# Performance work log

Measured on AMD Instinct MI355X. Metric: run time of the kernel, lower is better.

Reference implementation:

```python
import jax, jax.numpy as jnp
import numpy as np

EPS = 1e-5
CIN = [3, 24, 48, 96, 192]
COUT = [24, 48, 96, 192, 384]
P = 512
NUM_CLASSES = 101
FC_IN = 384 * 16 * 3 * 3  # 55296


def _poly_layer(x, proj, alpha, gamma, beta):
    # x: (B, C, D, H, W)
    B, C, D, H, W = x.shape
    # im2col: 3x3x3 patches with zero padding 1 -> (B, C*27, D, H, W)
    patches = jax.lax.conv_general_dilated_patches(
        x, filter_shape=(3, 3, 3), window_strides=(1, 1, 1),
        padding=[(1, 1), (1, 1), (1, 1)])
    patches = jnp.moveaxis(patches, 1, -1)  # (B, D, H, W, C*27)
    ws = jnp.einsum('bdhwk,pk->bdhwp', patches, proj)      # projector GEMM
    out = jnp.einsum('bdhwp,po->bdhwo', ws, alpha)         # alpha GEMM
    out = jnp.maximum(1.0 + out, 0.0)                      # clamp(1+x, min=0)
    out = jnp.moveaxis(out, -1, 1)                         # (B, O, D, H, W)
    # MaxPool3d kernel/stride (1,2,2)
    out = jax.lax.reduce_window(out, -jnp.inf, jax.lax.max,
                                (1, 1, 1, 2, 2), (1, 1, 1, 2, 2), 'VALID')
    # BatchNorm3d with batch statistics (train-mode math)
    mean = out.mean(axis=(0, 2, 3, 4), keepdims=True)
    var = out.var(axis=(0, 2, 3, 4), keepdims=True)
    out = (out - mean) * jax.lax.rsqrt(var + EPS)
    out = out * gamma.reshape(1, -1, 1, 1, 1) + beta.reshape(1, -1, 1, 1, 1)
    return out


def setup_inputs() -> dict:
    key = jax.random.key(0)
    keys = jax.random.split(key, 32)
    inp = {'x': jax.random.normal(keys[0], (2, 3, 16, 112, 112), dtype=jnp.float32)}
    ki = 1
    for i in range(5):
        k_feat = CIN[i] * 27
        inp[f'p{i+1}'] = jax.random.normal(keys[ki], (P, k_feat), dtype=jnp.float32) / np.sqrt(k_feat); ki += 1
        inp[f'a{i+1}'] = jax.random.normal(keys[ki], (P, COUT[i]), dtype=jnp.float32) * np.sqrt(2.0 / COUT[i]); ki += 1
        inp[f'g{i+1}'] = jnp.ones((COUT[i],), dtype=jnp.float32)
        inp[f'q{i+1}'] = jnp.zeros((COUT[i],), dtype=jnp.float32)
    inp['w1'] = jax.random.normal(keys[ki], (512, FC_IN), dtype=jnp.float32) * np.sqrt(2.0 / 512); ki += 1
    inp['b1'] = jnp.zeros((512,), dtype=jnp.float32)
    inp['w2'] = jax.random.normal(keys[ki], (256, 512), dtype=jnp.float32) * np.sqrt(2.0 / 256); ki += 1
    inp['b2'] = jnp.zeros((256,), dtype=jnp.float32)
    inp['w3'] = jax.random.normal(keys[ki], (NUM_CLASSES, 256), dtype=jnp.float32) * np.sqrt(2.0 / NUM_CLASSES); ki += 1
    inp['b3'] = jnp.zeros((NUM_CLASSES,), dtype=jnp.float32)
    return inp


def reference(x, p1, a1, g1, q1, p2, a2, g2, q2, p3, a3, g3, q3,
              p4, a4, g4, q4, p5, a5, g5, q5, w1, b1, w2, b2, w3, b3):
    projs = [p1, p2, p3, p4, p5]
    alphas = [a1, a2, a3, a4, a5]
    gammas = [g1, g2, g3, g4, g5]
    betas = [q1, q2, q3, q4, q5]
    h = x
    for i in range(5):
        h = _poly_layer(h, projs[i], alphas[i], gammas[i], betas[i])
    h = h.reshape(h.shape[0], -1)  # (B, 55296)
    h = jax.nn.relu(h @ w1.T + b1)  # dropout = identity (eval)
    h = jax.nn.relu(h @ w2.T + b2)
    logits = h @ w3.T + b3
    return logits
```

## Files before the change

### kernel.cpp

```cpp
#include <hip/hip_runtime.h>

#define EPS_BN 1e-5f

typedef __attribute__((ext_vector_type(8))) short sh8;
typedef __attribute__((ext_vector_type(4))) short sh4;
typedef __attribute__((ext_vector_type(4))) float f32x4;

static const size_t WF_OFF[5] = {0, 1944, 33048, 157464, 655128};
static const size_t PART_OFF = 2645784;
static const size_t PRE_OFF  = 6258456;
static const size_t OUT5_OFF = 8666904;
static const size_t H_OFF    = 8777496;
static const size_t ST_OFF   = 8888088;
static const size_t BNP_OFF  = 8888856;
static const size_t H1_OFF   = 8938008;
static const size_t WS_TOT   = 8939032;
__device__ __align__(256) float g_ws[WS_TOT];

static const size_t XIN_OFF = 0;
static const size_t A1_OFF  = 1871424;
static const size_t A2_OFF  = 4776768;
static const size_t A3_OFF  = 6331968;
static const size_t A4_OFF  = 7216704;
static const size_t AR_TOT  = 7776576;
__device__ __align__(256) unsigned short g_act[AR_TOT];

static const size_t WB_OFF[5] = {0, 4096, 36352, 162304, 659968};
__device__ __align__(256) unsigned short g_wb[2650624];

__device__ inline unsigned short f2bf(float v) {
    unsigned u = __float_as_uint(v);
    return (unsigned short)((u + 0x7fffu + ((u >> 16) & 1u)) >> 16);
}

__global__ __launch_bounds__(256) void init_input(const float* __restrict__ x,
                                                  unsigned short* __restrict__ xp,
                                                  float* __restrict__ bnp,
                                                  int4* __restrict__ zp, int nz)
{
    const int i = blockIdx.x * 256 + threadIdx.x;
    if (i < nz) zp[i] = make_int4(0, 0, 0, 0);
    if (i < 49152) bnp[i] = 0.f;
    if (i >= 2 * 18 * 114 * 114 * 4) return;
    const int c = i & 3;
    int t = i >> 2;
    const int xx = t % 114; t /= 114;
    const int yy = t % 114; t /= 114;
    const int zz = t % 18;
    const int b  = t / 18;
    float v = 0.f;
    if (c < 3 && (unsigned)(zz - 1) < 16u && (unsigned)(yy - 1) < 112u && (unsigned)(xx - 1) < 112u)
        v = x[(((size_t)b * 3 + c) * 16 + (zz - 1)) * 12544 + (yy - 1) * 112 + (xx - 1)];
    xp[i] = f2bf(v);
}

struct FuseArgs {
    const float* proj[5];
    const float* alpha[5];
    float* Wf[5];
    int K[5];
    int CO[5];
    int NT[5];
    int start[6];
};

__global__ __launch_bounds__(256) void fuse_all(FuseArgs a)
{
    __shared__ __align__(16) float sa[16][64];
    __shared__ __align__(16) float sp[16][64];

    int l = 0;
    {
        const int bx = blockIdx.x;
        while (l < 4 && bx >= a.start[l + 1]) ++l;
    }
    const int idx = blockIdx.x - a.start[l];
    const int NT = a.NT[l];
    const int obase = (idx / NT) * 64;
    const int kbase = (idx % NT) * 64;
    const int K = a.K[l], CO = a.CO[l];
    const float* __restrict__ proj  = a.proj[l];
    const float* __restrict__ alpha = a.alpha[l];
    float* __restrict__ Wf = a.Wf[l];

    const int tid = threadIdx.x;
    const int tk = tid & 15, to = tid >> 4;

    const int pp  = tid >> 4;
    const int col = (tid & 15) * 4;
    const int o_st = obase + col;
    const int k_st = kbase + col;
    const bool a_ok  = (o_st < CO);
    const bool p_vec = ((K & 3) == 0) && (k_st + 4 <= K);

    float acc[4][4];
    #pragma unroll
    for (int i = 0; i < 4; ++i)
        #pragma unroll
        for (int j = 0; j < 4; ++j) acc[i][j] = 0.f;

    for (int p0 = 0; p0 < 512; p0 += 16) {
        const float* ap  = alpha + (size_t)(p0 + pp) * CO;
        const float* prp = proj  + (size_t)(p0 + pp) * K;
        float4 va = make_float4(0.f, 0.f, 0.f, 0.f);
        float4 vp = make_float4(0.f, 0.f, 0.f, 0.f);
        if (a_ok) va = *(const float4*)(ap + o_st);
        if (p_vec) {
            vp = *(const float4*)(prp + k_st);
        } else {
            float t4[4];
            #pragma unroll
            for (int j = 0; j < 4; ++j)
                t4[j] = (k_st + j < K) ? prp[k_st + j] : 0.f;
            vp = make_float4(t4[0], t4[1], t4[2], t4[3]);
        }
        *(float4*)&sa[pp][col] = va;
        *(float4*)&sp[pp][col] = vp;
        __syncthreads();
        #pragma unroll
        for (int p = 0; p < 16; ++p) {
            const float4 a4 = *(const float4*)&sa[p][to * 4];
            const float4 b4 = *(const float4*)&sp[p][tk * 4];
            const float aa[4] = {a4.x, a4.y, a4.z, a4.w};
            const float bb[4] = {b4.x, b4.y, b4.z, b4.w};
            #pragma unroll
            for (int i = 0; i < 4; ++i)
                #pragma unroll
                for (int j = 0; j < 4; ++j)
                    acc[i][j] = fmaf(aa[i], bb[j], acc[i][j]);
        }
        __syncthreads();
    }

    #pragma unroll
    for (int i = 0; i < 4; ++i) {
        const int o = obase + to * 4 + i;
        if (o < CO) {
            #pragma unroll
            for (int j = 0; j < 4; ++j) {
                const int kk = kbase + tk * 4 + j;
                if (kk < K) Wf[(size_t)o * K + kk] = acc[i][j];
            }
        }
    }
}

struct ReordArgs {
    const float* Wf[5];
    unsigned short* Wb[5];
    int K[5], CPAD[5], KPAD[5], CO[5];
    int start[6];
};

__global__ __launch_bounds__(256) void reorder_all(ReordArgs a)
{
    int l = 0;
    {
        const int bx = blockIdx.x;
        while (l < 4 && bx >= a.start[l + 1]) ++l;
    }
    const int o = blockIdx.x - a.start[l];
    const int K = a.K[l], CPAD = a.CPAD[l], KPAD = a.KPAD[l], CO = a.CO[l];
    const int tid = threadIdx.x;
    unsigned short* row = a.Wb[l] + (size_t)o * KPAD;
    for (int i = tid; i < KPAD; i += 256) row[i] = 0;
    __syncthreads();
    if (o < CO) {
        const float* wr = a.Wf[l] + (size_t)o * K;
        for (int k = tid; k < K; k += 256) {
            const int c = k / 27, s = k - c * 27;
            row[s * CPAD + c] = f2bf(wr[k]);
        }
    }
}

template<int CPAD, int COUT, int KPAD, int HI, int WI, int HP, int WP, int NBLK, int SPLIT>
__global__ __launch_bounds__(256) void conv_mfma(
    const unsigned short* __restrict__ in, const unsigned short* __restrict__ Wb,
    float* __restrict__ outf, float* __restrict__ part, float* __restrict__ bnp)
{
    constexpr int NT = NBLK / 16;
    constexpr int HI2 = HI + 2, WI2 = WI + 2;
    constexpr bool C8 = (CPAD % 8 == 0);
    constexpr int TABN = C8 ? KPAD / 8 : KPAD / 4;
    constexpr int NSTEP = KPAD / 32 / SPLIT;
    constexpr int MTOT = 2 * 16 * HP * WP * 4;
    constexpr bool BONCE = (NBLK * KPAD * 2 <= 16384);
    constexpr int BROW = BONCE ? (KPAD + 8) : 40;
    constexpr int BS_ELEMS = BONCE ? NBLK * BROW : 2 * NBLK * 40;

    __shared__ __align__(16) unsigned short As[2][128 * 40];
    __shared__ __align__(16) unsigned short Bs[BS_ELEMS];
    __shared__ int tab[TABN];
    __shared__ float bs[(SPLIT == 1) ? 2 * NBLK : 1];

    const int tid = threadIdx.x;
    const int lane = tid & 63;
    const int wv = tid >> 6;
    const int blk_m = blockIdx.x;
    const int oc0 = blockIdx.y * NBLK;
    const int kc = (SPLIT > 1) ? blockIdx.z : 0;

    for (int i = tid; i < TABN; i += 256) {
        const int k = i * (C8 ? 8 : 4);
        const int s = k / CPAD, c = k % CPAD;
        tab[i] = (s < 27) ? ((((s / 9) * HI2 + (s % 9) / 3) * WI2 + (s % 3)) * CPAD + c) : -1;
    }

    if constexpr (BONCE) {
        for (int i = tid; i < NBLK * KPAD / 8; i += 256) {
            const int r = i / (KPAD / 8), kk = i - r * (KPAD / 8);
            *(sh8*)&Bs[r * BROW + kk * 8] = *(const sh8*)&Wb[(size_t)(oc0 + r) * KPAD + kk * 8];
        }
    }

    const int srow = tid >> 1;
    const int half = tid & 1;
    const int m_g = blk_m * 128 + srow;
    {
    }
    const int pooled_s = m_g >> 2, sub_s = m_g & 3;
    const int pw_g = pooled_s % WP;
    const int ph_g = (pooled_s / WP) % HP;
    const int d_g  = (pooled_s / (WP * HP)) & 15;
    const int b_g  = pooled_s / (WP * HP * 16);
    const int h_g = 2 * ph_g + (sub_s >> 1);
    const int w_g = 2 * pw_g + (sub_s & 1);
    const size_t base_m = ((((size_t)b_g * 18 + d_g) * HI2 + h_g) * WI2 + w_g) * CPAD;

    const int brow = tid >> 2, bcc = tid & 3;
    const bool bload = (tid < NBLK * 4);

    f32x4 acc[2][NT];
    #pragma unroll
    for (int mf = 0; mf < 2; ++mf)
        #pragma unroll
        for (int i = 0; i < NT; ++i) acc[mf][i] = (f32x4){0.f, 0.f, 0.f, 0.f};

    const int k_begin = kc * NSTEP * 32;

    sh8 aA0, aA1;
    sh4 aP0, aP1, aP2, aP3;
    sh8 brg;

    __syncthreads();

    {
        const int k0 = k_begin;
        if constexpr (C8) {
            const int o0 = tab[(k0 >> 3) + half * 2];
            const int o1 = tab[(k0 >> 3) + half * 2 + 1];
            aA0 = (sh8){0, 0, 0, 0, 0, 0, 0, 0};
            aA1 = (sh8){0, 0, 0, 0, 0, 0, 0, 0};
            if (o0 >= 0) aA0 = *(const sh8*)(in + base_m + o0);
            if (o1 >= 0) aA1 = *(const sh8*)(in + base_m + o1);
            *(sh8*)&As[0][srow * 40 + (half * 2) * 8]     = aA0;
            *(sh8*)&As[0][srow * 40 + (half * 2 + 1) * 8] = aA1;
        } else {
            const int t0 = tab[(k0 >> 2) + half * 4];
            const int t1 = tab[(k0 >> 2) + half * 4 + 1];
            const int t2 = tab[(k0 >> 2) + half * 4 + 2];
            const int t3 = tab[(k0 >> 2) + half * 4 + 3];
            aP0 = (sh4){0, 0, 0, 0}; aP1 = (sh4){0, 0, 0, 0};
            aP2 = (sh4){0, 0, 0, 0}; aP3 = (sh4){0, 0, 0, 0};
            if (t0 >= 0) aP0 = *(const sh4*)(in + base_m + t0);
            if (t1 >= 0) aP1 = *(const sh4*)(in + base_m + t1);
            if (t2 >= 0) aP2 = *(const sh4*)(in + base_m + t2);
            if (t3 >= 0) aP3 = *(const sh4*)(in + base_m + t3);
            *(sh4*)&As[0][srow * 40 + (half * 4) * 4]     = aP0;
            *(sh4*)&As[0][srow * 40 + (half * 4 + 1) * 4] = aP1;
            *(sh4*)&As[0][srow * 40 + (half * 4 + 2) * 4] = aP2;
            *(sh4*)&As[0][srow * 40 + (half * 4 + 3) * 4] = aP3;
        }
        if constexpr (!BONCE) {
            if (bload) {
                brg = *(const sh8*)&Wb[(size_t)(oc0 + brow) * KPAD + k0 + bcc * 8];
                *(sh8*)&Bs[0 + brow * 40 + bcc * 8] = brg;
            }
        }
    }
    __syncthreads();

    int cur = 0;
    for (int s = 0; s < NSTEP; ++s) {
        const int k0 = k_begin + s * 32;
        if (s + 1 < NSTEP) {
            const int kn = k0 + 32;
            if constexpr (C8) {
                const int o0 = tab[(kn >> 3) + half * 2];
                const int o1 = tab[(kn >> 3) + half * 2 + 1];
                aA0 = (sh8){0, 0, 0, 0, 0, 0, 0, 0};
                aA1 = (sh8){0, 0, 0, 0, 0, 0, 0, 0};
                if (o0 >= 0) aA0 = *(const sh8*)(in + base_m + o0);
                if (o1 >= 0) aA1 = *(const sh8*)(in + base_m + o1);
            } else {
                const int t0 = tab[(kn >> 2) + half * 4];
                const int t1 = tab[(kn >> 2) + half * 4 + 1];
                const int t2 = tab[(kn >> 2) + half * 4 + 2];
                const int t3 = tab[(kn >> 2) + half * 4 + 3];
                aP0 = (sh4){0, 0, 0, 0}; aP1 = (sh4){0, 0, 0, 0};
                aP2 = (sh4){0, 0, 0, 0}; aP3 = (sh4){0, 0, 0, 0};
                if (t0 >= 0) aP0 = *(const sh4*)(in + base_m + t0);
                if (t1 >= 0) aP1 = *(const sh4*)(in + base_m + t1);
                if (t2 >= 0) aP2 = *(const sh4*)(in + base_m + t2);
                if (t3 >= 0) aP3 = *(const sh4*)(in + base_m + t3);
            }
            if constexpr (!BONCE) {
                if (bload) brg = *(const sh8*)&Wb[(size_t)(oc0 + brow) * KPAD + kn + bcc * 8];
            }
        }
        const sh8 af0 = *(const sh8*)&As[cur][(wv * 16 + (lane & 15)) * 40 + (lane >> 4) * 8];
        const sh8 af1 = *(const sh8*)&As[cur][(64 + wv * 16 + (lane & 15)) * 40 + (lane >> 4) * 8];
        #pragma unroll
        for (int nt = 0; nt < NT; ++nt) {
            sh8 bf;
            if constexpr (BONCE)
                bf = *(const sh8*)&Bs[(nt * 16 + (lane & 15)) * BROW + k0 + (lane >> 4) * 8];
            else
                bf = *(const sh8*)&Bs[cur * NBLK * 40 + (nt * 16 + (lane & 15)) * 40 + (lane >> 4) * 8];
            acc[0][nt] = __builtin_amdgcn_mfma_f32_16x16x32_bf16(af0, bf, acc[0][nt], 0, 0, 0);
            acc[1][nt] = __builtin_amdgcn_mfma_f32_16x16x32_bf16(af1, bf, acc[1][nt], 0, 0, 0);
        }
        if (s + 1 < NSTEP) {
            if constexpr (C8) {
                *(sh8*)&As[cur ^ 1][srow * 40 + (half * 2) * 8]     = aA0;
                *(sh8*)&As[cur ^ 1][srow * 40 + (half * 2 + 1) * 8] = aA1;
            } else {
                *(sh4*)&As[cur ^ 1][srow * 40 + (half * 4) * 4]     = aP0;
                *(sh4*)&As[cur ^ 1][srow * 40 + (half * 4 + 1) * 4] = aP1;
                *(sh4*)&As[cur ^ 1][srow * 40 + (half * 4 + 2) * 4] = aP2;
                *(sh4*)&As[cur ^ 1][srow * 40 + (half * 4 + 3) * 4] = aP3;
            }
            if constexpr (!BONCE) {
                if (bload) *(sh8*)&Bs[(cur ^ 1) * NBLK * 40 + brow * 40 + bcc * 8] = brg;
            }
        }
        __syncthreads();
        cur ^= 1;
    }

    const int q = lane >> 4;
    const int nloc = lane & 15;
    if constexpr (SPLIT == 1) {
        for (int i = tid; i < 2 * NBLK; i += 256) bs[i] = 0.f;
        __syncthreads();
        #pragma unroll
        for (int mf = 0; mf < 2; ++mf) {
            const int pooled_o = blk_m * 32 + mf * 16 + wv * 4 + q;
            #pragma unroll
            for (int nt = 0; nt < NT; ++nt) {
                const int oc = oc0 + nt * 16 + nloc;
                float mx = fmaxf(1.f + acc[mf][nt][0], 0.f);
                mx = fmaxf(mx, fmaxf(1.f + acc[mf][nt][1], 0.f));
                mx = fmaxf(mx, fmaxf(1.f + acc[mf][nt][2], 0.f));
                mx = fmaxf(mx, fmaxf(1.f + acc[mf][nt][3], 0.f));
                float s1 = 0.f;
                if (oc < COUT) {
                    outf[(size_t)pooled_o * COUT + oc] = mx;
                    s1 = mx;
                }
                float s2 = s1 * s1;
                s1 += __shfl_xor(s1, 16);
                s1 += __shfl_xor(s1, 32);
                s2 += __shfl_xor(s2, 16);
                s2 += __shfl_xor(s2, 32);
                if (q == 0) {
                    atomicAdd(&bs[nt * 16 + nloc], s1);
                    atomicAdd(&bs[NBLK + nt * 16 + nloc], s2);
                }
            }
        }
        __syncthreads();
        float* rowp = bnp + (size_t)(blk_m & 63) * 768;
        for (int i = tid; i < NBLK; i += 256) {
            const int oc = oc0 + i;
            if (oc < COUT) {
                atomicAdd(&rowp[oc], bs[i]);
                atomicAdd(&rowp[384 + oc], bs[NBLK + i]);
            }
        }
    } else {
        #pragma unroll
        for (int mf = 0; mf < 2; ++mf) {
            #pragma unroll
            for (int nt = 0; nt < NT; ++nt) {
                const int oc = oc0 + nt * 16 + nloc;
                #pragma unroll
                for (int r = 0; r < 4; ++r) {
                    const int mm = blk_m * 128 + mf * 64 + wv * 16 + q * 4 + r;
                    part[((size_t)kc * MTOT + mm) * COUT + oc] = acc[mf][nt][r];
                }
            }
        }
    }
}

template<int COUT, int HP, int WP, int SPLIT>
__global__ __launch_bounds__(256) void pool_epi(const float* __restrict__ part,
                                                float* __restrict__ outf,
                                                float* __restrict__ bnp)
{
    constexpr int PO = 2 * 16 * HP * WP;
    constexpr int M = PO * 4;
    __shared__ float bs[2 * COUT];
    const int tid = threadIdx.x;
    for (int i = tid; i < 2 * COUT; i += 256) bs[i] = 0.f;
    __syncthreads();
    const int idx = blockIdx.x * 256 + tid;
    if (idx < PO * COUT) {
        const int oc = idx % COUT;
        const int p = idx / COUT;
        float v[4] = {0.f, 0.f, 0.f, 0.f};
        for (int s = 0; s < SPLIT; ++s)
            #pragma unroll
            for (int r = 0; r < 4; ++r)
                v[r] += part[((size_t)s * M + p * 4 + r) * COUT + oc];
        float mx = fmaxf(1.f + v[0], 0.f);
        mx = fmaxf(mx, fmaxf(1.f + v[1], 0.f));
        mx = fmaxf(mx, fmaxf(1.f + v[2], 0.f));
        mx = fmaxf(mx, fmaxf(1.f + v[3], 0.f));
        outf[(size_t)p * COUT + oc] = mx;
        atomicAdd(&bs[oc], mx);
        atomicAdd(&bs[COUT + oc], mx * mx);
    }
    __syncthreads();
    float* rowp = bnp + (size_t)(blockIdx.x & 63) * 768;
    for (int i = tid; i < COUT; i += 256) {
        atomicAdd(&rowp[i], bs[i]);
        atomicAdd(&rowp[384 + i], bs[COUT + i]);
    }
}

__global__ __launch_bounds__(64) void bn_reduce(float* __restrict__ bnp,
                                                const float* __restrict__ gamma,
                                                const float* __restrict__ beta,
                                                float* __restrict__ st,
                                                float inv_n)
{
    const int c = blockIdx.x, tid = threadIdx.x;
    float s = bnp[(size_t)tid * 768 + c];
    float q = bnp[(size_t)tid * 768 + 384 + c];
    bnp[(size_t)tid * 768 + c] = 0.f;
    bnp[(size_t)tid * 768 + 384 + c] = 0.f;
    #pragma unroll
    for (int off = 32; off > 0; off >>= 1) {
        s += __shfl_down(s, off);
        q += __shfl_down(q, off);
    }
    if (tid == 0) {
        const float mean = s * inv_n;
        const float var  = q * inv_n - mean * mean;
        const float sc   = gamma[c] * rsqrtf(var + EPS_BN);
        st[2 * c]     = sc;
        st[2 * c + 1] = fmaf(-mean, sc, beta[c]);
    }
}

template<int C, int HP, int WP>
__global__ __launch_bounds__(256) void bn_apply_halo(const float* __restrict__ pre,
                                                     const float* __restrict__ st,
                                                     unsigned short* __restrict__ outh)
{
    constexpr int PO = 2 * 16 * HP * WP;
    const int idx = blockIdx.x * 256 + threadIdx.x;
    if (idx >= PO * C) return;
    const int c = idx % C;
    const int p = idx / C;
    const int pw = p % WP;
    const int ph = (p / WP) % HP;
    const int d  = (p / (WP * HP)) & 15;
    const int b  = p / (WP * HP * 16);
    const float v = fmaf(pre[idx], st[2 * c], st[2 * c + 1]);
    outh[((((size_t)b * 18 + d + 1) * (HP + 2) + ph + 1) * (WP + 2) + pw + 1) * C + c] = f2bf(v);
}

__global__ __launch_bounds__(256) void transpose5(const float* __restrict__ out5,
                                                  const float* __restrict__ st,
                                                  float* __restrict__ h)
{
    const int idx = blockIdx.x * 256 + threadIdx.x;
    if (idx >= 110592) return;
    const int c = idx % 384;
    const int p = idx / 384;
    const int b = p / 144;
    const int sp = p % 144;
    h[(size_t)b * 55296 + c * 144 + sp] = fmaf(out5[idx], st[2 * c], st[2 * c + 1]);
}

__global__ __launch_bounds__(256) void fc1_k(const float* __restrict__ h,
                                             const float* __restrict__ w1,
                                             const float* __restrict__ b1,
                                             float* __restrict__ hout)
{
    __shared__ float r0[256];
    __shared__ float r1[256];
    const int j = blockIdx.x, tid = threadIdx.x;
    const float* wr = w1 + (size_t)j * 55296;
    float a0 = 0.f, a1 = 0.f;
    for (int k = tid * 4; k < 55296; k += 1024) {
        const float4 w = *(const float4*)(wr + k);
        const float4 u = *(const float4*)(h + k);
        const float4 v = *(const float4*)(h + 55296 + k);
        a0 += w.x * u.x + w.y * u.y + w.z * u.z + w.w * u.w;
        a1 += w.x * v.x + w.y * v.y + w.z * v.z + w.w * v.w;
    }
    r0[tid] = a0; r1[tid] = a1;
    __syncthreads();
    for (int off = 128; off > 0; off >>= 1) {
        if (tid < off) { r0[tid] += r0[tid + off]; r1[tid] += r1[tid + off]; }
        __syncthreads();
    }
    if (tid == 0) {
        hout[j]       = fmaxf(r0[0] + b1[j], 0.f);
        hout[512 + j] = fmaxf(r1[0] + b1[j], 0.f);
    }
}

__global__ __launch_bounds__(256) void fc23_k(const float* __restrict__ h1,
                                              const float* __restrict__ w2,
                                              const float* __restrict__ b2,
                                              const float* __restrict__ w3,
                                              const float* __restrict__ b3,
                                              float* __restrict__ out)
{
    __shared__ float h1s[1024];
    __shared__ float h2[512];
    const int tid = threadIdx.x;
    for (int i = tid; i < 1024; i += 256) h1s[i] = h1[i];
    __syncthreads();
    {
        const float* wr = w2 + (size_t)tid * 512;
        #pragma unroll
        for (int b = 0; b < 2; ++b) {
            float a = 0.f;
            const float* hh = h1s + b * 512;
            for (int k = 0; k < 512; ++k) a = fmaf(wr[k], hh[k], a);
            h2[b * 256 + tid] = fmaxf(a + b2[tid], 0.f);
        }
    }
    __syncthreads();
    if (tid < 101) {
        const float* wr = w3 + (size_t)tid * 256;
        #pragma unroll
        for (int b = 0; b < 2; ++b) {
            float a = 0.f;
            const float* hh = h2 + b * 256;
            for (int k = 0; k < 256; ++k) a = fmaf(wr[k], hh[k], a);
            out[b * 101 + tid] = a + b3[tid];
        }
    }
}

extern "C" void kernel_launch(void* const* d_in, const int* in_sizes, int n_in,
                              void* d_out, int out_size, void* d_ws, size_t ws_size,
                              hipStream_t stream)
{
    const float* x  = (const float*)d_in[0];
    const float* p[5], *al[5], *g[5], *q[5];
    for (int i = 0; i < 5; ++i) {
        p[i]  = (const float*)d_in[1 + 4 * i];
        al[i] = (const float*)d_in[2 + 4 * i];
        g[i]  = (const float*)d_in[3 + 4 * i];
        q[i]  = (const float*)d_in[4 + 4 * i];
    }
    const float* w1 = (const float*)d_in[21];
    const float* b1 = (const float*)d_in[22];
    const float* w2 = (const float*)d_in[23];
    const float* b2 = (const float*)d_in[24];
    const float* w3 = (const float*)d_in[25];
    const float* b3 = (const float*)d_in[26];

    float* ws = nullptr;
    hipGetSymbolAddress((void**)&ws, HIP_SYMBOL(g_ws));
    unsigned short* act = nullptr;
    hipGetSymbolAddress((void**)&act, HIP_SYMBOL(g_act));
    unsigned short* wb = nullptr;
    hipGetSymbolAddress((void**)&wb, HIP_SYMBOL(g_wb));

    float* Wf[5];
    for (int i = 0; i < 5; ++i) Wf[i] = ws + WF_OFF[i];
    float* part = ws + PART_OFF;
    float* pre  = ws + PRE_OFF;
    float* out5 = ws + OUT5_OFF;
    float* h    = ws + H_OFF;
    float* st   = ws + ST_OFF;
    float* bnp  = ws + BNP_OFF;
    float* h1   = ws + H1_OFF;

    unsigned short* xin = act + XIN_OFF;
    unsigned short* a1  = act + A1_OFF;
    unsigned short* a2  = act + A2_OFF;
    unsigned short* a3  = act + A3_OFF;
    unsigned short* a4  = act + A4_OFF;

    {
        const int nz = (int)((AR_TOT - A1_OFF) * 2 / 16);
        init_input<<<(2 * 18 * 114 * 114 * 4 + 255) / 256, 256, 0, stream>>>(
            x, xin, bnp, (int4*)(act + A1_OFF), nz);
    }

    static const int KF[5] = {81, 648, 1296, 2592, 5184};
    static const int CO[5] = {24, 48, 96, 192, 384};
    static const int CP[5] = {4, 24, 48, 96, 192};
    static const int KP[5] = {128, 672, 1312, 2592, 5184};
    static const int NPAD[5] = {32, 48, 96, 192, 384};

    FuseArgs fa;
    int s0 = 0;
    for (int i = 0; i < 5; ++i) {
        fa.proj[i] = p[i]; fa.alpha[i] = al[i]; fa.Wf[i] = Wf[i];
        fa.K[i] = KF[i]; fa.CO[i] = CO[i];
        const int nt = (KF[i] + 63) / 64;
        const int mt = (CO[i] + 63) / 64;
        fa.NT[i] = nt;
        fa.start[i] = s0;
        s0 += nt * mt;
    }
    fa.start[5] = s0;
    fuse_all<<<s0, 256, 0, stream>>>(fa);

    ReordArgs ra;
    int r0 = 0;
    for (int i = 0; i < 5; ++i) {
        ra.Wf[i] = Wf[i]; ra.Wb[i] = wb + WB_OFF[i];
        ra.K[i] = KF[i]; ra.CPAD[i] = CP[i]; ra.KPAD[i] = KP[i]; ra.CO[i] = CO[i];
        ra.start[i] = r0;
        r0 += NPAD[i];
    }
    ra.start[5] = r0;
    reorder_all<<<r0, 256, 0, stream>>>(ra);

    conv_mfma<4, 24, 128, 112, 112, 56, 56, 32, 1>
        <<<dim3(3136, 1), 256, 0, stream>>>(xin, wb + WB_OFF[0], pre, nullptr, bnp);
    bn_reduce<<<24, 64, 0, stream>>>(bnp, g[0], q[0], st, 1.f / 100352.f);
    bn_apply_halo<24, 56, 56><<<9408, 256, 0, stream>>>(pre, st, a1);

    conv_mfma<24, 48, 672, 56, 56, 28, 28, 48, 1>
        <<<dim3(784, 1), 256, 0, stream>>>(a1, wb + WB_OFF[1], pre, nullptr, bnp);
    bn_reduce<<<48, 64, 0, stream>>>(bnp, g[1], q[1], st, 1.f / 25088.f);
    bn_apply_halo<48, 28, 28><<<4704, 256, 0, stream>>>(pre, st, a2);

    conv_mfma<48, 96, 1312, 28, 28, 14, 14, 48, 1>
        <<<dim3(196, 2), 256, 0, stream>>>(a2, wb + WB_OFF[2], pre, nullptr, bnp);
    bn_reduce<<<96, 64, 0, stream>>>(bnp, g[2], q[2], st, 1.f / 6272.f);
    bn_apply_halo<96, 14, 14><<<2352, 256, 0, stream>>>(pre, st, a3);

    conv_mfma<96, 192, 2592, 14, 14, 7, 7, 64, 3>
        <<<dim3(49, 3, 3), 256, 0, stream>>>(a3, wb + WB_OFF[3], nullptr, part, bnp);
    pool_epi<192, 7, 7, 3><<<1176, 256, 0, stream>>>(part, pre, bnp);
    bn_reduce<<<192, 64, 0, stream>>>(bnp, g[3], q[3], st, 1.f / 1568.f);
    bn_apply_halo<192, 7, 7><<<1176, 256, 0, stream>>>(pre, st, a4);

    conv_mfma<192, 384, 5184, 7, 7, 3, 3, 64, 6>
        <<<dim3(9, 6, 6), 256, 0, stream>>>(a4, wb + WB_OFF[4], nullptr, part, bnp);
    pool_epi<384, 3, 3, 6><<<432, 256, 0, stream>>>(part, out5, bnp);
    bn_reduce<<<384, 64, 0, stream>>>(bnp, g[4], q[4], st, 1.f / 288.f);

    transpose5<<<(110592 + 255) / 256, 256, 0, stream>>>(out5, st, h);
    fc1_k<<<512, 256, 0, stream>>>(h, w1, b1, h1);
    fc23_k<<<1, 256, 0, stream>>>(h1, w2, b2, w3, b3, (float*)d_out);
}
```

Measured before the change: 514.0 us.

## Fuse projector/alpha weights with split-bf16 MFMA and drop reorder pass

Replaces the scalar FP32 fuse GEMM (alpha^T x proj) and the separate reorder kernel with a transpose/split kernel and a bf16 MFMA fuse kernel. The transpose kernel writes each weight into high and low bf16 parts. The MFMA kernel computes the product with three MFMAs (hi*hi, hi*lo, lo*hi) to keep near-FP32 accuracy, then writes bf16 weights directly in the conv layout. Zeroing of the weight buffer moves into init_input. The aim is to cut the FP32 ALU cost of weight preparation and one kernel launch, in exchange for an extra transposed staging buffer and a small precision change.

```diff
diff --git a/kernel.cpp b/kernel.cpp
--- a/kernel.cpp
+++ b/kernel.cpp
@@ -6,7 +6,6 @@
 typedef __attribute__((ext_vector_type(4))) short sh4;
 typedef __attribute__((ext_vector_type(4))) float f32x4;
 
-static const size_t WF_OFF[5] = {0, 1944, 33048, 157464, 655128};
 static const size_t PART_OFF = 2645784;
 static const size_t PRE_OFF  = 6258456;
 static const size_t OUT5_OFF = 8666904;
@@ -26,20 +25,26 @@
 __device__ __align__(256) unsigned short g_act[AR_TOT];
 
 static const size_t WB_OFF[5] = {0, 4096, 36352, 162304, 659968};
-__device__ __align__(256) unsigned short g_wb[2650624];
+static const size_t WB_TOT    = 2650624;
+__device__ __align__(256) unsigned short g_wb[WB_TOT];
 
 __device__ inline unsigned short f2bf(float v) {
     unsigned u = __float_as_uint(v);
     return (unsigned short)((u + 0x7fffu + ((u >> 16) & 1u)) >> 16);
 }
+__device__ inline float bf2f(unsigned short h) {
+    return __uint_as_float(((unsigned)h) << 16);
+}
 
 __global__ __launch_bounds__(256) void init_input(const float* __restrict__ x,
                                                   unsigned short* __restrict__ xp,
                                                   float* __restrict__ bnp,
-                                                  int4* __restrict__ zp, int nz)
+                                                  int4* __restrict__ zp, int nz,
+                                                  int4* __restrict__ wbz, int nwb)
 {
     const int i = blockIdx.x * 256 + threadIdx.x;
     if (i < nz) zp[i] = make_int4(0, 0, 0, 0);
+    if (i < nwb) wbz[i] = make_int4(0, 0, 0, 0);
     if (i < 49152) bnp[i] = 0.f;
     if (i >= 2 * 18 * 114 * 114 * 4) return;
     const int c = i & 3;
@@ -54,122 +59,115 @@
     xp[i] = f2bf(v);
 }
 
-struct FuseArgs {
-    const float* proj[5];
-    const float* alpha[5];
-    float* Wf[5];
-    int K[5];
-    int CO[5];
-    int NT[5];
+struct PrepArgs {
+    const float* src[10];
+    int W[10];
+    int dstrow[10];
+    int start[11];
+    int rowtot;
+};
+
+__global__ __launch_bounds__(256) void prep_t(PrepArgs a, unsigned short* __restrict__ dst)
+{
+    __shared__ unsigned short tileh[32 * 72];
+    __shared__ unsigned short tilel[32 * 72];
+    int m = 0;
+    {
+        const int bx = blockIdx.x;
+        while (m < 9 && bx >= a.start[m + 1]) ++m;
+    }
+    const int t  = blockIdx.x - a.start[m];
+    const int tw = t >> 4, tp = t & 15;
+    const int p0 = tp * 32, w0 = tw * 64;
+    const int W = a.W[m];
+    const float* __restrict__ src = a.src[m];
+    const int tid = threadIdx.x;
+
+    #pragma unroll
+    for (int e = 0; e < 8; ++e) {
+        const int idx = tid + e * 256;
+        const int w = idx & 63, pr = idx >> 6;
+        const int gw = w0 + w;
+        float v = 0.f;
+        if (gw < W) v = src[(size_t)(p0 + pr) * W + gw];
+        const unsigned short hh = f2bf(v);
+        tileh[pr * 72 + w] = hh;
+        tilel[pr * 72 + w] = f2bf(v - bf2f(hh));
+    }
+    __syncthreads();
+    {
+        const int wr = tid >> 2, pg = (tid & 3) * 8;
+        sh8 packh, packl;
+        #pragma unroll
+        for (int e = 0; e < 8; ++e) {
+            packh[e] = (short)tileh[(pg + e) * 72 + wr];
+            packl[e] = (short)tilel[(pg + e) * 72 + wr];
+        }
+        const size_t rh = (size_t)a.dstrow[m] + w0 + wr;
+        *(sh8*)&dst[rh * 512 + p0 + pg] = packh;
+        *(sh8*)&dst[(rh + a.rowtot) * 512 + p0 + pg] = packl;
+    }
+}
+
+struct Fuse2Args {
+    int aoff[5], poff[5];
+    int wboff[5];
+    int K[5], CO[5], KPAD[5], CPAD[5];
+    int kt[5];
     int start[6];
+    int rowtot;
 };
 
-__global__ __launch_bounds__(256) void fuse_all(FuseArgs a)
-{
-    __shared__ __align__(16) float sa[16][64];
-    __shared__ __align__(16) float sp[16][64];
-
+__global__ __launch_bounds__(256) void fuse_mfma(const unsigned short* __restrict__ tb,
+                                                 unsigned short* __restrict__ wb,
+                                                 Fuse2Args a)
+{
     int l = 0;
     {
         const int bx = blockIdx.x;
         while (l < 4 && bx >= a.start[l + 1]) ++l;
     }
     const int idx = blockIdx.x - a.start[l];
-    const int NT = a.NT[l];
-    const int obase = (idx / NT) * 64;
-    const int kbase = (idx % NT) * 64;
-    const int K = a.K[l], CO = a.CO[l];
-    const float* __restrict__ proj  = a.proj[l];
-    const float* __restrict__ alpha = a.alpha[l];
-    float* __restrict__ Wf = a.Wf[l];
-
-    const int tid = threadIdx.x;
-    const int tk = tid & 15, to = tid >> 4;
-
-    const int pp  = tid >> 4;
-    const int col = (tid & 15) * 4;
-    const int o_st = obase + col;
-    const int k_st = kbase + col;
-    const bool a_ok  = (o_st < CO);
-    const bool p_vec = ((K & 3) == 0) && (k_st + 4 <= K);
-
-    float acc[4][4];
+    const int ot = idx / a.kt[l];
+    const int kt = idx % a.kt[l];
+    const int lane = threadIdx.x & 63;
+    const int wv = threadIdx.x >> 6;
+    const size_t LOFF = (size_t)a.rowtot * 512;
+
+    const unsigned short* arow = tb + ((size_t)(a.aoff[l] + ot * 64 + wv * 16 + (lane & 15))) * 512 + (lane >> 4) * 8;
+    const unsigned short* brow = tb + ((size_t)(a.poff[l] + kt * 64 + (lane & 15))) * 512 + (lane >> 4) * 8;
+
+    f32x4 acc[4];
     #pragma unroll
-    for (int i = 0; i < 4; ++i)
-        #pragma unroll
-        for (int j = 0; j < 4; ++j) acc[i][j] = 0.f;
-
-    for (int p0 = 0; p0 < 512; p0 += 16) {
-        const float* ap  = alpha + (size_t)(p0 + pp) * CO;
-        const float* prp = proj  + (size_t)(p0 + pp) * K;
-        float4 va = make_float4(0.f, 0.f, 0.f, 0.f);
-        float4 vp = make_float4(0.f, 0.f, 0.f, 0.f);
-        if (a_ok) va = *(const float4*)(ap + o_st);
-        if (p_vec) {
-            vp = *(const float4*)(prp + k_st);
-        } else {
-            float t4[4];
-            #pragma unroll
-            for (int j = 0; j < 4; ++j)
-                t4[j] = (k_st + j < K) ? prp[k_st + j] : 0.f;
-            vp = make_float4(t4[0], t4[1], t4[2], t4[3]);
-        }
-        *(float4*)&sa[pp][col] = va;
-        *(float4*)&sp[pp][col] = vp;
-        __syncthreads();
-        #pragma unroll
-        for (int p = 0; p < 16; ++p) {
-            const float4 a4 = *(const float4*)&sa[p][to * 4];
-            const float4 b4 = *(const float4*)&sp[p][tk * 4];
-            const float aa[4] = {a4.x, a4.y, a4.z, a4.w};
-            const float bb[4] = {b4.x, b4.y, b4.z, b4.w};
-            #pragma unroll
-            for (int i = 0; i < 4; ++i)
-                #pragma unroll
-                for (int j = 0; j < 4; ++j)
-                    acc[i][j] = fmaf(aa[i], bb[j], acc[i][j]);
-        }
-        __syncthreads();
-    }
-
+    for (int i = 0; i < 4; ++i) acc[i] = (f32x4){0.f, 0.f, 0.f, 0.f};
+
+    #pragma unroll 2
+    for (int p0 = 0; p0 < 512; p0 += 32) {
+        const sh8 afh = *(const sh8*)(arow + p0);
+        const sh8 afl = *(const sh8*)(arow + LOFF + p0);
+        #pragma unroll
+        for (int nt = 0; nt < 4; ++nt) {
+            const sh8 bfh = *(const sh8*)(brow + (size_t)nt * 16 * 512 + p0);
+            const sh8 bfl = *(const sh8*)(brow + LOFF + (size_t)nt * 16 * 512 + p0);
+            acc[nt] = __builtin_amdgcn_mfma_f32_16x16x32_bf16(afh, bfh, acc[nt], 0, 0, 0);
+            acc[nt] = __builtin_amdgcn_mfma_f32_16x16x32_bf16(afh, bfl, acc[nt], 0, 0, 0);
+            acc[nt] = __builtin_amdgcn_mfma_f32_16x16x32_bf16(afl, bfh, acc[nt], 0, 0, 0);
+        }
+    }
+
+    const int K = a.K[l], CO = a.CO[l], KP = a.KPAD[l], CP = a.CPAD[l];
+    unsigned short* wbl = wb + a.wboff[l];
     #pragma unroll
-    for (int i = 0; i < 4; ++i) {
-        const int o = obase + to * 4 + i;
-        if (o < CO) {
+    for (int nt = 0; nt < 4; ++nt) {
+        const int kk = kt * 64 + nt * 16 + (lane & 15);
+        if (kk < K) {
+            const int c = kk / 27, s = kk - c * 27;
+            const int col = s * CP + c;
             #pragma unroll
             for (int j = 0; j < 4; ++j) {
-                const int kk = kbase + tk * 4 + j;
-                if (kk < K) Wf[(size_t)o * K + kk] = acc[i][j];
-            }
-        }
-    }
-}
-
-struct ReordArgs {
-    const float* Wf[5];
-    unsigned short* Wb[5];
-    int K[5], CPAD[5], KPAD[5], CO[5];
-    int start[6];
-};
-
-__global__ __launch_bounds__(256) void reorder_all(ReordArgs a)
-{
-    int l = 0;
-    {
-        const int bx = blockIdx.x;
-        while (l < 4 && bx >= a.start[l + 1]) ++l;
-    }
-    const int o = blockIdx.x - a.start[l];
-    const int K = a.K[l], CPAD = a.CPAD[l], KPAD = a.KPAD[l], CO = a.CO[l];
-    const int tid = threadIdx.x;
-    unsigned short* row = a.Wb[l] + (size_t)o * KPAD;
-    for (int i = tid; i < KPAD; i += 256) row[i] = 0;
-    __syncthreads();
-    if (o < CO) {
-        const float* wr = a.Wf[l] + (size_t)o * K;
-        for (int k = tid; k < K; k += 256) {
-            const int c = k / 27, s = k - c * 27;
-            row[s * CPAD + c] = f2bf(wr[k]);
+                const int o = ot * 64 + wv * 16 + (lane >> 4) * 4 + j;
+                if (o < CO) wbl[(size_t)o * KP + col] = f2bf(acc[nt][j]);
+            }
         }
     }
 }
@@ -217,8 +215,6 @@
     const int srow = tid >> 1;
     const int half = tid & 1;
     const int m_g = blk_m * 128 + srow;
-    {
-    }
     const int pooled_s = m_g >> 2, sub_s = m_g & 3;
     const int pw_g = pooled_s % WP;
     const int ph_g = (pooled_s / WP) % HP;
@@ -577,8 +573,6 @@
     unsigned short* wb = nullptr;
     hipGetSymbolAddress((void**)&wb, HIP_SYMBOL(g_wb));
 
-    float* Wf[5];
-    for (int i = 0; i < 5; ++i) Wf[i] = ws + WF_OFF[i];
     float* part = ws + PART_OFF;
     float* pre  = ws + PRE_OFF;
     float* out5 = ws + OUT5_OFF;
@@ -586,6 +580,7 @@
     float* st   = ws + ST_OFF;
     float* bnp  = ws + BNP_OFF;
     float* h1   = ws + H1_OFF;
+    unsigned short* tbuf = (unsigned short*)(ws + PART_OFF);
 
     unsigned short* xin = act + XIN_OFF;
     unsigned short* a1  = act + A1_OFF;
@@ -593,42 +588,60 @@
     unsigned short* a3  = act + A3_OFF;
     unsigned short* a4  = act + A4_OFF;
 
-    {
-        const int nz = (int)((AR_TOT - A1_OFF) * 2 / 16);
-        init_input<<<(2 * 18 * 114 * 114 * 4 + 255) / 256, 256, 0, stream>>>(
-            x, xin, bnp, (int4*)(act + A1_OFF), nz);
-    }
-
     static const int KF[5] = {81, 648, 1296, 2592, 5184};
     static const int CO[5] = {24, 48, 96, 192, 384};
     static const int CP[5] = {4, 24, 48, 96, 192};
     static const int KP[5] = {128, 672, 1312, 2592, 5184};
-    static const int NPAD[5] = {32, 48, 96, 192, 384};
-
-    FuseArgs fa;
-    int s0 = 0;
-    for (int i = 0; i < 5; ++i) {
-        fa.proj[i] = p[i]; fa.alpha[i] = al[i]; fa.Wf[i] = Wf[i];
-        fa.K[i] = KF[i]; fa.CO[i] = CO[i];
-        const int nt = (KF[i] + 63) / 64;
-        const int mt = (CO[i] + 63) / 64;
-        fa.NT[i] = nt;
-        fa.start[i] = s0;
-        s0 += nt * mt;
-    }
-    fa.start[5] = s0;
-    fuse_all<<<s0, 256, 0, stream>>>(fa);
-
-    ReordArgs ra;
-    int r0 = 0;
-    for (int i = 0; i < 5; ++i) {
-        ra.Wf[i] = Wf[i]; ra.Wb[i] = wb + WB_OFF[i];
-        ra.K[i] = KF[i]; ra.CPAD[i] = CP[i]; ra.KPAD[i] = KP[i]; ra.CO[i] = CO[i];
-        ra.start[i] = r0;
-        r0 += NPAD[i];
-    }
-    ra.start[5] = r0;
-    reorder_all<<<r0, 256, 0, stream>>>(ra);
+    static const int APAD[5] = {64, 64, 128, 192, 384};
+    static const int PPAD[5] = {128, 704, 1344, 2624, 5184};
+    static const int KT[5] = {2, 11, 21, 41, 81};
+    static const int OT[5] = {1, 1, 2, 3, 6};
+
+    {
+        const int nz = (int)((AR_TOT - A1_OFF) * 2 / 16);
+        const int nwb = (int)(WB_TOT * 2 / 16);
+        init_input<<<(2 * 18 * 114 * 114 * 4 + 255) / 256, 256, 0, stream>>>(
+            x, xin, bnp, (int4*)(act + A1_OFF), nz, (int4*)wb, nwb);
+    }
+
+    PrepArgs pa;
+    Fuse2Args f2;
+    int rowtot = 0;
+    {
+        int row = 0, blk = 0;
+        pa.start[0] = 0;
+        for (int i = 0; i < 5; ++i) {
+            pa.src[i] = al[i]; pa.W[i] = CO[i]; pa.dstrow[i] = row;
+            f2.aoff[i] = row;
+            row += APAD[i];
+            blk += (APAD[i] / 64) * 16;
+            pa.start[i + 1] = blk;
+        }
+        for (int i = 0; i < 5; ++i) {
+            pa.src[5 + i] = p[i]; pa.W[5 + i] = KF[i]; pa.dstrow[5 + i] = row;
+            f2.poff[i] = row;
+            row += PPAD[i];
+            blk += (PPAD[i] / 64) * 16;
+            pa.start[5 + i + 1] = blk;
+        }
+        rowtot = row;
+        pa.rowtot = rowtot;
+        f2.rowtot = rowtot;
+        prep_t<<<blk, 256, 0, stream>>>(pa, tbuf);
+    }
+
+    {
+        int s0 = 0;
+        for (int i = 0; i < 5; ++i) {
+            f2.wboff[i] = (int)WB_OFF[i];
+            f2.K[i] = KF[i]; f2.CO[i] = CO[i]; f2.KPAD[i] = KP[i]; f2.CPAD[i] = CP[i];
+            f2.kt[i] = KT[i];
+            f2.start[i] = s0;
+            s0 += KT[i] * OT[i];
+        }
+        f2.start[5] = s0;
+        fuse_mfma<<<s0, 256, 0, stream>>>(tbuf, wb, f2);
+    }
 
     conv_mfma<4, 24, 128, 112, 112, 56, 56, 32, 1>
         <<<dim3(3136, 1), 256, 0, stream>>>(xin, wb + WB_OFF[0], pre, nullptr, bnp);
```

Measured after the change: 542.4 us. 1.06x slower.
